# Kernel optimization log

Hardware: AMD Instinct MI355X
Metric: run time of the kernel (lower is better)

The kernel has to match this reference:

```python
import jax, jax.numpy as jnp
import numpy as np

B, M = 64, 2048
D_LLM = 4096
D_T, D_P, D_C = 256, 512, 1024
NH_T, NH_P, NH_C = 4, 8, 16
S_T, S_P, S_C = 4, 8, 4
LN_EPS = 1e-5


def setup_inputs() -> dict:
    key = jax.random.key(0)
    ks = iter(jax.random.split(key, 48))
    def n(shape, s=0.02):
        return jax.random.normal(next(ks), shape, jnp.float32) * s
    inp = {
        "hidden_state": jax.random.normal(next(ks), (B, D_LLM), jnp.float32),
        "time_fiber": jax.random.normal(next(ks), (M, D_T), jnp.float32),
        "topic_fiber": jax.random.normal(next(ks), (M, D_P), jnp.float32),
        "ctx_fiber": jax.random.normal(next(ks), (M, D_C), jnp.float32),
        "mem_mask": jnp.zeros((B, M), bool),
        # BundleQueryHeads: Linear(d_LLM -> d_F_*) per bundle (torch weight layout (out,in))
        "Wq_time": n((D_T, D_LLM)), "bq_time": jnp.zeros((D_T,), jnp.float32),
        "Wq_topic": n((D_P, D_LLM)), "bq_topic": jnp.zeros((D_P,), jnp.float32),
        "Wq_ctx": n((D_C, D_LLM)), "bq_ctx": jnp.zeros((D_C,), jnp.float32),
        # nn.MultiheadAttention packed in_proj (3d, d) and out_proj (d, d)
        "Wqkv_time": n((3 * D_T, D_T)), "bqkv_time": jnp.zeros((3 * D_T,), jnp.float32),
        "Wo_time": n((D_T, D_T)), "bo_time": jnp.zeros((D_T,), jnp.float32),
        "Wqkv_topic": n((3 * D_P, D_P)), "bqkv_topic": jnp.zeros((3 * D_P,), jnp.float32),
        "Wo_topic": n((D_P, D_P)), "bo_topic": jnp.zeros((D_P,), jnp.float32),
        "Wqkv_ctx": n((3 * D_C, D_C)), "bqkv_ctx": jnp.zeros((3 * D_C,), jnp.float32),
        "Wo_ctx": n((D_C, D_C)), "bo_ctx": jnp.zeros((D_C,), jnp.float32),
        # per-slot lifts stacked: (slots, d_F, d_LLM) for einsum 'bd,sde->bse'
        "Wlift_time": n((S_T, D_T, D_LLM)), "blift_time": jnp.zeros((S_T, D_LLM), jnp.float32),
        "Wlift_topic": n((S_P, D_P, D_LLM)), "blift_topic": jnp.zeros((S_P, D_LLM), jnp.float32),
        "Wlift_ctx": n((S_C, D_C, D_LLM)), "blift_ctx": jnp.zeros((S_C, D_LLM), jnp.float32),
        "ln_g": jnp.ones((D_LLM,), jnp.float32),
        "ln_b": jnp.zeros((D_LLM,), jnp.float32),
    }
    return inp


def _mha1(q, kv, Wqkv, bqkv, Wo, bo, nh, mask):
    """Single-query-token MHA. q: (B,d); kv: (M,d) shared across batch; mask: (B,M) True=ignore."""
    d = q.shape[-1]
    hd = d // nh
    Wq, Wk, Wv = jnp.split(Wqkv, 3, axis=0)
    bq, bk, bv = jnp.split(bqkv, 3, axis=0)
    qp = (q @ Wq.T + bq).reshape(-1, nh, hd)    # (B,h,hd)
    kp = (kv @ Wk.T + bk).reshape(-1, nh, hd)   # (M,h,hd)
    vp = (kv @ Wv.T + bv).reshape(-1, nh, hd)   # (M,h,hd)
    scale = 1.0 / np.float32(np.sqrt(hd))
    scores = jnp.einsum('bhd,mhd->bhm', qp, kp) * scale  # (B,h,M)
    scores = jnp.where(mask[:, None, :], jnp.float32(-1e9), scores)
    attn = jax.nn.softmax(scores, axis=-1)
    out = jnp.einsum('bhm,mhd->bhd', attn, vp).reshape(-1, d)  # (B,d)
    return out @ Wo.T + bo


def _layernorm(x, g, b):
    mu = jnp.mean(x, axis=-1, keepdims=True)
    var = jnp.mean((x - mu) ** 2, axis=-1, keepdims=True)
    return (x - mu) * jax.lax.rsqrt(var + LN_EPS) * g + b


def reference(hidden_state, time_fiber, topic_fiber, ctx_fiber, mem_mask,
              Wq_time, bq_time, Wq_topic, bq_topic, Wq_ctx, bq_ctx,
              Wqkv_time, bqkv_time, Wo_time, bo_time,
              Wqkv_topic, bqkv_topic, Wo_topic, bo_topic,
              Wqkv_ctx, bqkv_ctx, Wo_ctx, bo_ctx,
              Wlift_time, blift_time, Wlift_topic, blift_topic, Wlift_ctx, blift_ctx,
              ln_g, ln_b):
    # bundle query heads
    q_time = hidden_state @ Wq_time.T + bq_time
    q_topic = hidden_state @ Wq_topic.T + bq_topic
    q_ctx = hidden_state @ Wq_ctx.T + bq_ctx
    # three single-token cross attentions
    o_time = _mha1(q_time, time_fiber, Wqkv_time, bqkv_time, Wo_time, bo_time, NH_T, mem_mask)
    o_topic = _mha1(q_topic, topic_fiber, Wqkv_topic, bqkv_topic, Wo_topic, bo_topic, NH_P, mem_mask)
    o_ctx = _mha1(q_ctx, ctx_fiber, Wqkv_ctx, bqkv_ctx, Wo_ctx, bo_ctx, NH_C, mem_mask)
    # per-slot lifts, batched across slots
    slots_time = jnp.einsum('bd,sde->bse', o_time, Wlift_time) + blift_time[None]
    slots_topic = jnp.einsum('bd,sde->bse', o_topic, Wlift_topic) + blift_topic[None]
    slots_ctx = jnp.einsum('bd,sde->bse', o_ctx, Wlift_ctx) + blift_ctx[None]
    prefix = jnp.concatenate([slots_time, slots_topic, slots_ctx], axis=1)  # (B, L_mem, d_LLM)
    return _layernorm(prefix, ln_g, ln_b)
```

## Files before the change

### kernel.cpp

```cpp
#include <hip/hip_runtime.h>
#include <cstdint>
#include <cstddef>

typedef __attribute__((ext_vector_type(8))) short short8;
typedef __attribute__((ext_vector_type(4))) float floatx4;

__device__ __forceinline__ unsigned short f2bf(float f) {
    unsigned int u = __builtin_bit_cast(unsigned int, f);
    u += 0x7fffu + ((u >> 16) & 1u);
    return (unsigned short)(u >> 16);
}
__device__ __forceinline__ float bflo(unsigned int u) {
    return __builtin_bit_cast(float, u << 16);
}
__device__ __forceinline__ short8 pack8(float4 a, float4 b) {
    short8 r;
    r[0] = (short)f2bf(a.x); r[1] = (short)f2bf(a.y);
    r[2] = (short)f2bf(a.z); r[3] = (short)f2bf(a.w);
    r[4] = (short)f2bf(b.x); r[5] = (short)f2bf(b.y);
    r[6] = (short)f2bf(b.z); r[7] = (short)f2bf(b.w);
    return r;
}

struct SubGemm {
    const float* A; const float* W; const float* bias;
    float* Cf; unsigned short* Ch;
    int K, N, Kc, nj, ni, nkz, mode, ldc;
};
struct GemmBatch { SubGemm d[16]; int start[16]; int nd; };

__global__ __launch_bounds__(256) void gemm_batch(GemmBatch gb)
{
    __shared__ short As[2][64 * 40];
    __shared__ __align__(16) char Braw[2][32 * 132 * 4];

    const int bx = blockIdx.x;
    int di = 0;
#pragma unroll 1
    for (int i = 1; i < gb.nd; ++i) if (bx >= gb.start[i]) di = i;
    const SubGemm g = gb.d[di];
    int local = bx - gb.start[di];
    const int jb = local % g.nj; local /= g.nj;
    const int ib = local % g.ni;
    const int kz = local / g.ni;

    const int tid = threadIdx.x;
    const int w = tid >> 6, lane = tid & 63;
    const int quad = lane >> 4, l16 = lane & 15;
    const int noff = w * 32;

    const int rA = tid >> 2, cA = (tid & 3) * 8;
    const float* pa = g.A + (size_t)(ib * 64 + rA) * g.K + kz * g.Kc + cA;

    floatx4 acc[4][2] = {};

    if (g.mode <= 1) {
        const int rB = tid >> 1, cB = (tid & 1) * 16;
        const float* pb = g.W + (size_t)(jb * 128 + rB) * g.K + kz * g.Kc + cB;
        float4 a0 = *(const float4*)(pa), a1 = *(const float4*)(pa + 4);
        float4 b0 = *(const float4*)(pb),     b1 = *(const float4*)(pb + 4);
        float4 b2 = *(const float4*)(pb + 8), b3 = *(const float4*)(pb + 12);
        {
            short* Asp = As[0]; short* Bsp = (short*)Braw[0];
            *(short8*)&Asp[rA * 40 + cA]     = pack8(a0, a1);
            *(short8*)&Bsp[rB * 40 + cB]     = pack8(b0, b1);
            *(short8*)&Bsp[rB * 40 + cB + 8] = pack8(b2, b3);
        }
        if (g.Kc > 32) {
            pa += 32; pb += 32;
            a0 = *(const float4*)(pa);     a1 = *(const float4*)(pa + 4);
            b0 = *(const float4*)(pb);     b1 = *(const float4*)(pb + 4);
            b2 = *(const float4*)(pb + 8); b3 = *(const float4*)(pb + 12);
        }
        int cur = 0;
#pragma unroll 1
        for (int k0 = 0; k0 < g.Kc; k0 += 32) {
            __syncthreads();
            const short* Asc = As[cur];
            const short* Bsc = (const short*)Braw[cur];
            short8 af[4], bfr[2];
#pragma unroll
            for (int r = 0; r < 4; ++r)
                af[r] = *(const short8*)&Asc[(r * 16 + l16) * 40 + quad * 8];
#pragma unroll
            for (int c = 0; c < 2; ++c)
                bfr[c] = *(const short8*)&Bsc[(noff + c * 16 + l16) * 40 + quad * 8];
#pragma unroll
            for (int r = 0; r < 4; ++r)
#pragma unroll
                for (int c = 0; c < 2; ++c)
                    acc[r][c] = __builtin_amdgcn_mfma_f32_16x16x32_bf16(af[r], bfr[c], acc[r][c], 0, 0, 0);
            if (k0 + 32 < g.Kc) {
                short* Asn = As[cur ^ 1]; short* Bsn = (short*)Braw[cur ^ 1];
                *(short8*)&Asn[rA * 40 + cA]     = pack8(a0, a1);
                *(short8*)&Bsn[rB * 40 + cB]     = pack8(b0, b1);
                *(short8*)&Bsn[rB * 40 + cB + 8] = pack8(b2, b3);
                if (k0 + 64 < g.Kc) {
                    pa += 32; pb += 32;
                    a0 = *(const float4*)(pa);     a1 = *(const float4*)(pa + 4);
                    b0 = *(const float4*)(pb);     b1 = *(const float4*)(pb + 4);
                    b2 = *(const float4*)(pb + 8); b3 = *(const float4*)(pb + 12);
                }
            }
            cur ^= 1;
        }
    } else {
        const int rK = tid >> 3, cN = (tid & 7) * 16;
        const int cNs = cN ^ ((rK & 8) << 1);
        const float* pb = g.W + (size_t)(kz * g.Kc + rK) * g.N + jb * 128 + cN;
        float4 a0 = *(const float4*)(pa), a1 = *(const float4*)(pa + 4);
        float4 b0 = *(const float4*)(pb),     b1 = *(const float4*)(pb + 4);
        float4 b2 = *(const float4*)(pb + 8), b3 = *(const float4*)(pb + 12);
        {
            short* Asp = As[0]; float* Bp = (float*)Braw[0];
            *(short8*)&Asp[rA * 40 + cA] = pack8(a0, a1);
            *(float4*)&Bp[rK * 132 + cNs]      = b0;
            *(float4*)&Bp[rK * 132 + cNs + 4]  = b1;
            *(float4*)&Bp[rK * 132 + cNs + 8]  = b2;
            *(float4*)&Bp[rK * 132 + cNs + 12] = b3;
        }
        if (g.Kc > 32) {
            pa += 32; pb += (size_t)32 * g.N;
            a0 = *(const float4*)(pa);     a1 = *(const float4*)(pa + 4);
            b0 = *(const float4*)(pb);     b1 = *(const float4*)(pb + 4);
            b2 = *(const float4*)(pb + 8); b3 = *(const float4*)(pb + 12);
        }
        int cur = 0;
#pragma unroll 1
        for (int k0 = 0; k0 < g.Kc; k0 += 32) {
            __syncthreads();
            const short* Asc = As[cur];
            const float* Bc = (const float*)Braw[cur];
            short8 af[4], bfr[2];
#pragma unroll
            for (int r = 0; r < 4; ++r)
                af[r] = *(const short8*)&Asc[(r * 16 + l16) * 40 + quad * 8];
#pragma unroll
            for (int c = 0; c < 2; ++c) {
                const int colb = (noff + c * 16 + l16) ^ ((quad & 1) << 4);
#pragma unroll
                for (int i = 0; i < 8; ++i)
                    bfr[c][i] = (short)f2bf(Bc[(quad * 8 + i) * 132 + colb]);
            }
#pragma unroll
            for (int r = 0; r < 4; ++r)
#pragma unroll
                for (int c = 0; c < 2; ++c)
                    acc[r][c] = __builtin_amdgcn_mfma_f32_16x16x32_bf16(af[r], bfr[c], acc[r][c], 0, 0, 0);
            if (k0 + 32 < g.Kc) {
                short* Asn = As[cur ^ 1]; float* Bn = (float*)Braw[cur ^ 1];
                *(short8*)&Asn[rA * 40 + cA] = pack8(a0, a1);
                *(float4*)&Bn[rK * 132 + cNs]      = b0;
                *(float4*)&Bn[rK * 132 + cNs + 4]  = b1;
                *(float4*)&Bn[rK * 132 + cNs + 8]  = b2;
                *(float4*)&Bn[rK * 132 + cNs + 12] = b3;
                if (k0 + 64 < g.Kc) {
                    pa += 32; pb += (size_t)32 * g.N;
                    a0 = *(const float4*)(pa);     a1 = *(const float4*)(pa + 4);
                    b0 = *(const float4*)(pb);     b1 = *(const float4*)(pb + 4);
                    b2 = *(const float4*)(pb + 8); b3 = *(const float4*)(pb + 12);
                }
            }
            cur ^= 1;
        }
    }

#pragma unroll
    for (int r = 0; r < 4; ++r)
#pragma unroll
        for (int c = 0; c < 2; ++c) {
            const int col = jb * 128 + noff + c * 16 + l16;
            const float bj = (g.bias == nullptr) ? 0.f
                           : ((g.mode == 1 && kz != 0) ? 0.f : g.bias[col]);
#pragma unroll
            for (int q = 0; q < 4; ++q) {
                const int row = ib * 64 + r * 16 + quad * 4 + q;
                const float v = acc[r][c][q] + bj;
                if (g.mode == 0)
                    g.Ch[(size_t)row * g.ldc + col] = f2bf(v);
                else if (g.mode == 1) {
                    if (g.nkz > 1) atomicAdd(&g.Cf[(size_t)row * g.ldc + col], v);
                    else           g.Cf[(size_t)row * g.ldc + col] = v;
                } else {
                    if (g.nkz > 1) atomicAdd(&g.Cf[(size_t)row * g.ldc + col], v);
                    else           g.Cf[(size_t)row * g.ldc + col] = v;
                }
            }
        }
}

__global__ __launch_bounds__(256) void qk_batch(
    const float* __restrict__ qp_t, const float* __restrict__ qp_p, const float* __restrict__ qp_c,
    const unsigned short* __restrict__ kv_t, const unsigned short* __restrict__ kv_p, const unsigned short* __restrict__ kv_c,
    float* __restrict__ S_t, float* __restrict__ S_p, float* __restrict__ S_c)
{
    __shared__ short As[64 * 72];
    __shared__ short Bs[128 * 72];
    const int hy = blockIdx.y;
    const float* qp; const unsigned short* kv; float* S; int d, h;
    if (hy < 4)       { qp = qp_t; kv = kv_t; S = S_t; d = 256;  h = hy; }
    else if (hy < 12) { qp = qp_p; kv = kv_p; S = S_p; d = 512;  h = hy - 4; }
    else              { qp = qp_c; kv = kv_c; S = S_c; d = 1024; h = hy - 12; }

    const int j0 = blockIdx.x * 128;
    const int tid = threadIdx.x;
    const int w = tid >> 6, lane = tid & 63;
    const int quad = lane >> 4, l16 = lane & 15;
    const int noff = w * 32;
    const int twoD = 2 * d;

    {
        const int b = tid >> 2, kc = (tid & 3) * 16;
        const float* ga = qp + (size_t)b * d + h * 64 + kc;
        float4 a0 = *(const float4*)(ga + 0), a1 = *(const float4*)(ga + 4);
        float4 a2 = *(const float4*)(ga + 8), a3 = *(const float4*)(ga + 12);
        *(short8*)&As[b * 72 + kc + 0] = pack8(a0, a1);
        *(short8*)&As[b * 72 + kc + 8] = pack8(a2, a3);
    }
    {
        const int m = tid >> 1, hf = (tid & 1) * 32;
        const unsigned short* gb = kv + (size_t)(j0 + m) * twoD + h * 64 + hf;
        uint4 b0 = *(const uint4*)(gb + 0),  b1 = *(const uint4*)(gb + 8);
        uint4 b2 = *(const uint4*)(gb + 16), b3 = *(const uint4*)(gb + 24);
        *(uint4*)&Bs[m * 72 + hf + 0]  = b0;
        *(uint4*)&Bs[m * 72 + hf + 8]  = b1;
        *(uint4*)&Bs[m * 72 + hf + 16] = b2;
        *(uint4*)&Bs[m * 72 + hf + 24] = b3;
    }
    __syncthreads();

    floatx4 acc[4][2] = {};
#pragma unroll
    for (int k0 = 0; k0 < 64; k0 += 32) {
        short8 af[4], bfr[2];
#pragma unroll
        for (int r = 0; r < 4; ++r)
            af[r] = *(const short8*)&As[(r * 16 + l16) * 72 + k0 + quad * 8];
#pragma unroll
        for (int c = 0; c < 2; ++c)
            bfr[c] = *(const short8*)&Bs[(noff + c * 16 + l16) * 72 + k0 + quad * 8];
#pragma unroll
        for (int r = 0; r < 4; ++r)
#pragma unroll
            for (int c = 0; c < 2; ++c)
                acc[r][c] = __builtin_amdgcn_mfma_f32_16x16x32_bf16(af[r], bfr[c], acc[r][c], 0, 0, 0);
    }
#pragma unroll
    for (int r = 0; r < 4; ++r)
#pragma unroll
        for (int c = 0; c < 2; ++c) {
            int col = j0 + noff + c * 16 + l16;
#pragma unroll
            for (int q = 0; q < 4; ++q) {
                int row = r * 16 + quad * 4 + q;
                S[((size_t)h * 64 + row) * 2048 + col] = acc[r][c][q] * 0.125f;
            }
        }
}

__global__ __launch_bounds__(256) void softmax_pv_batch(
    const float* __restrict__ S_t, const float* __restrict__ S_p, const float* __restrict__ S_c,
    const unsigned short* __restrict__ kv_t, const unsigned short* __restrict__ kv_p, const unsigned short* __restrict__ kv_c,
    const uint8_t* __restrict__ mask,
    float* __restrict__ o_t, float* __restrict__ o_p, float* __restrict__ o_c)
{
    const int hy = blockIdx.x, b = blockIdx.y;
    const float* S; const unsigned short* kv; float* o; int d, h;
    if (hy < 4)       { S = S_t; kv = kv_t; o = o_t; d = 256;  h = hy; }
    else if (hy < 12) { S = S_p; kv = kv_p; o = o_p; d = 512;  h = hy - 4; }
    else              { S = S_c; kv = kv_c; o = o_c; d = 1024; h = hy - 12; }

    const int tid = threadIdx.x;
    __shared__ __align__(16) float sc[2048];
    __shared__ float red[4];
    __shared__ float part[4][64];
    __shared__ float s_max, s_sum;

    const float* Sr = S + ((size_t)h * 64 + b) * 2048;
    const uint8_t* mr = mask + (size_t)b * 2048;

    float lmax = -1e30f;
    for (int m = tid; m < 2048; m += 256) {
        float s = Sr[m];
        if (mr[m]) s = -1e9f;
        sc[m] = s;
        lmax = fmaxf(lmax, s);
    }
#pragma unroll
    for (int off = 32; off; off >>= 1) lmax = fmaxf(lmax, __shfl_down(lmax, off));
    if ((tid & 63) == 0) red[tid >> 6] = lmax;
    __syncthreads();
    if (tid == 0) s_max = fmaxf(fmaxf(red[0], red[1]), fmaxf(red[2], red[3]));
    __syncthreads();
    const float mx = s_max;

    float lsum = 0.f;
    for (int m = tid; m < 2048; m += 256) {
        float e = __expf(sc[m] - mx);
        sc[m] = e;
        lsum += e;
    }
#pragma unroll
    for (int off = 32; off; off >>= 1) lsum += __shfl_down(lsum, off);
    if ((tid & 63) == 0) red[tid >> 6] = lsum;
    __syncthreads();
    if (tid == 0) s_sum = red[0] + red[1] + red[2] + red[3];
    __syncthreads();

    const int lane = tid & 63, w = tid >> 6;
    const int twoD = 2 * d;
    const unsigned short* vcol = kv + d + h * 64 + lane;
    float acc = 0.f;
    const int m0 = w * 512;
#pragma unroll 1
    for (int m = m0; m < m0 + 512; m += 8) {
#pragma unroll
        for (int j = 0; j < 8; ++j)
            acc += sc[m + j] * bflo((unsigned int)vcol[(size_t)(m + j) * twoD]);
    }
    part[w][lane] = acc;
    __syncthreads();
    if (tid < 64) {
        float r = (part[0][tid] + part[1][tid] + part[2][tid] + part[3][tid]) / s_sum;
        o[(size_t)b * d + h * 64 + tid] = r;
    }
}

__global__ __launch_bounds__(256) void ln_kernel(
    float* __restrict__ x, const float* __restrict__ g, const float* __restrict__ bb,
    const float* __restrict__ blt, const float* __restrict__ blp, const float* __restrict__ blc)
{
    const int row = blockIdx.x;
    const int l = row & 15;
    const float* lb = (l < 4)  ? (blt + (size_t)l * 4096)
                    : (l < 12) ? (blp + (size_t)(l - 4) * 4096)
                               : (blc + (size_t)(l - 12) * 4096);
    float* xr = x + (size_t)row * 4096;
    const int tid = threadIdx.x;
    float v[16];
    float sum = 0.f, sumsq = 0.f;
#pragma unroll
    for (int i = 0; i < 16; ++i) {
        int e = tid + i * 256;
        v[i] = xr[e] + lb[e];
        sum += v[i];
        sumsq += v[i] * v[i];
    }
    __shared__ float rs[4], rq[4];
#pragma unroll
    for (int off = 32; off; off >>= 1) {
        sum += __shfl_down(sum, off);
        sumsq += __shfl_down(sumsq, off);
    }
    if ((tid & 63) == 0) { rs[tid >> 6] = sum; rq[tid >> 6] = sumsq; }
    __syncthreads();
    const float ts = rs[0] + rs[1] + rs[2] + rs[3];
    const float tq = rq[0] + rq[1] + rq[2] + rq[3];
    const float mu = ts * (1.f / 4096.f);
    const float var = tq * (1.f / 4096.f) - mu * mu;
    const float r = rsqrtf(var + 1e-5f);
#pragma unroll
    for (int i = 0; i < 16; ++i) {
        int e = tid + i * 256;
        xr[e] = (v[i] - mu) * r * g[e] + bb[e];
    }
}

static void addg(GemmBatch& G, int& tot,
                 const float* A, const float* W, const float* bias,
                 float* Cf, unsigned short* Ch,
                 int K, int N, int Kc, int nj, int ni, int nkz, int mode, int ldc)
{
    SubGemm& s = G.d[G.nd];
    s.A = A; s.W = W; s.bias = bias; s.Cf = Cf; s.Ch = Ch;
    s.K = K; s.N = N; s.Kc = Kc; s.nj = nj; s.ni = ni; s.nkz = nkz;
    s.mode = mode; s.ldc = ldc;
    G.start[G.nd] = tot;
    tot += nj * ni * nkz;
    G.nd++;
}

extern "C" void kernel_launch(void* const* d_in, const int* in_sizes, int n_in,
                              void* d_out, int out_size, void* d_ws, size_t ws_size,
                              hipStream_t stream)
{
    const float*   hs     = (const float*)d_in[0];
    const float*   fib_t  = (const float*)d_in[1];
    const float*   fib_p  = (const float*)d_in[2];
    const float*   fib_c  = (const float*)d_in[3];
    const uint8_t* mask   = (const uint8_t*)d_in[4];
    const float* Wq_t   = (const float*)d_in[5];  const float* bq_t   = (const float*)d_in[6];
    const float* Wq_p   = (const float*)d_in[7];  const float* bq_p   = (const float*)d_in[8];
    const float* Wq_c   = (const float*)d_in[9];  const float* bq_c   = (const float*)d_in[10];
    const float* Wqkv_t = (const float*)d_in[11]; const float* bqkv_t = (const float*)d_in[12];
    const float* Wo_t   = (const float*)d_in[13]; const float* bo_t   = (const float*)d_in[14];
    const float* Wqkv_p = (const float*)d_in[15]; const float* bqkv_p = (const float*)d_in[16];
    const float* Wo_p   = (const float*)d_in[17]; const float* bo_p   = (const float*)d_in[18];
    const float* Wqkv_c = (const float*)d_in[19]; const float* bqkv_c = (const float*)d_in[20];
    const float* Wo_c   = (const float*)d_in[21]; const float* bo_c   = (const float*)d_in[22];
    const float* Wl_t   = (const float*)d_in[23]; const float* bl_t   = (const float*)d_in[24];
    const float* Wl_p   = (const float*)d_in[25]; const float* bl_p   = (const float*)d_in[26];
    const float* Wl_c   = (const float*)d_in[27]; const float* bl_c   = (const float*)d_in[28];
    const float* ln_g   = (const float*)d_in[29]; const float* ln_b   = (const float*)d_in[30];

    char* wsb = (char*)d_ws;
    float* q_t  = (float*)wsb; wsb += 64 * 256 * 4;
    float* q_p  = (float*)wsb; wsb += 64 * 512 * 4;
    float* q_c  = (float*)wsb; wsb += 64 * 1024 * 4;
    float* qp_t = (float*)wsb; wsb += 64 * 256 * 4;
    float* qp_p = (float*)wsb; wsb += 64 * 512 * 4;
    float* qp_c = (float*)wsb; wsb += 64 * 1024 * 4;
    float* po_t = (float*)wsb; wsb += 64 * 256 * 4;
    float* po_p = (float*)wsb; wsb += 64 * 512 * 4;
    float* po_c = (float*)wsb; wsb += 64 * 1024 * 4;
    size_t zbytes = (size_t)(wsb - (char*)d_ws);
    float* o_t  = (float*)wsb; wsb += 64 * 256 * 4;
    float* o_p  = (float*)wsb; wsb += 64 * 512 * 4;
    float* o_c  = (float*)wsb; wsb += 64 * 1024 * 4;
    unsigned short* kv_t = (unsigned short*)wsb; wsb += 2048 * 512 * 2;
    unsigned short* kv_p = (unsigned short*)wsb; wsb += 2048 * 1024 * 2;
    unsigned short* kv_c = (unsigned short*)wsb; wsb += 2048 * 2048 * 2;
    float* S_t = (float*)wsb; wsb += (size_t)4  * 64 * 2048 * 4;
    float* S_p = (float*)wsb; wsb += (size_t)8  * 64 * 2048 * 4;
    float* S_c = (float*)wsb; wsb += (size_t)16 * 64 * 2048 * 4;
    float* out = (float*)d_out;

    const dim3 blk(256);
    hipMemsetAsync(d_ws, 0, zbytes, stream);
    hipMemsetAsync(d_out, 0, (size_t)out_size, stream);

    {
        GemmBatch G{}; int tot = 0; G.nd = 0;
        addg(G, tot, fib_c, Wqkv_c + 1024 * 1024, bqkv_c + 1024, nullptr, kv_c, 1024, 2048, 1024, 16, 32, 1, 0, 2048);
        addg(G, tot, fib_p, Wqkv_p + 512 * 512,   bqkv_p + 512,  nullptr, kv_p, 512,  1024, 512,  8,  32, 1, 0, 1024);
        addg(G, tot, fib_t, Wqkv_t + 256 * 256,   bqkv_t + 256,  nullptr, kv_t, 256,  512,  256,  4,  32, 1, 0, 512);
        addg(G, tot, hs, Wq_c, bq_c, q_c, nullptr, 4096, 1024, 256, 8, 1, 16, 1, 1024);
        addg(G, tot, hs, Wq_p, bq_p, q_p, nullptr, 4096, 512,  256, 4, 1, 16, 1, 512);
        addg(G, tot, hs, Wq_t, bq_t, q_t, nullptr, 4096, 256,  256, 2, 1, 16, 1, 256);
        gemm_batch<<<dim3(tot), blk, 0, stream>>>(G);
    }

    {
        GemmBatch G{}; int tot = 0; G.nd = 0;
        addg(G, tot, q_c, Wqkv_c, bqkv_c, qp_c, nullptr, 1024, 1024, 128, 8, 1, 8, 1, 1024);
        addg(G, tot, q_p, Wqkv_p, bqkv_p, qp_p, nullptr, 512,  512,  64,  4, 1, 8, 1, 512);
        addg(G, tot, q_t, Wqkv_t, bqkv_t, qp_t, nullptr, 256,  256,  64,  2, 1, 4, 1, 256);
        gemm_batch<<<dim3(tot), blk, 0, stream>>>(G);
    }

    qk_batch<<<dim3(16, 28), blk, 0, stream>>>(qp_t, qp_p, qp_c, kv_t, kv_p, kv_c, S_t, S_p, S_c);
    softmax_pv_batch<<<dim3(28, 64), blk, 0, stream>>>(S_t, S_p, S_c, kv_t, kv_p, kv_c, mask, o_t, o_p, o_c);

    {
        GemmBatch G{}; int tot = 0; G.nd = 0;
        addg(G, tot, o_c, Wo_c, bo_c, po_c, nullptr, 1024, 1024, 128, 8, 1, 8, 1, 1024);
        addg(G, tot, o_p, Wo_p, bo_p, po_p, nullptr, 512,  512,  64,  4, 1, 8, 1, 512);
        addg(G, tot, o_t, Wo_t, bo_t, po_t, nullptr, 256,  256,  64,  2, 1, 4, 1, 256);
        gemm_batch<<<dim3(tot), blk, 0, stream>>>(G);
    }

    {
        GemmBatch G{}; int tot = 0; G.nd = 0;
        for (int z = 0; z < 4; ++z)
            addg(G, tot, po_c, Wl_c + (size_t)z * 1024 * 4096, nullptr,
                 out + (size_t)(12 + z) * 4096, nullptr, 1024, 4096, 256, 32, 1, 4, 2, 16 * 4096);
        for (int z = 0; z < 8; ++z)
            addg(G, tot, po_p, Wl_p + (size_t)z * 512 * 4096, nullptr,
                 out + (size_t)(4 + z) * 4096, nullptr, 512, 4096, 256, 32, 1, 2, 2, 16 * 4096);
        for (int z = 0; z < 4; ++z)
            addg(G, tot, po_t, Wl_t + (size_t)z * 256 * 4096, nullptr,
                 out + (size_t)z * 4096, nullptr, 256, 4096, 256, 32, 1, 1, 2, 16 * 4096);
        gemm_batch<<<dim3(tot), blk, 0, stream>>>(G);
    }

    ln_kernel<<<dim3(1024), blk, 0, stream>>>(out, ln_g, ln_b, bl_t, bl_p, bl_c);
}
```

Baseline: 402.0 us.

## Split KV projection into 128x128 tiled GEMM and load B fragments directly to registers

The KV projection of the fibers moves out of the batched 64x128 GEMM into a dedicated 128x128-tile kernel with XOR-swizzled LDS, which doubles operand reuse per block. The thin GEMMs (query heads, in/out projections, lifts) no longer stage the weight matrix through shared memory. Each lane loads its B fragment straight from global memory into registers, with two-step software pipelining, which drops the B LDS traffic and its padding. The trade-offs are uncoalesced strided global loads for the transposed-weight mode, an extra kernel launch, and more registers per thread.

Measured after the change: 407.1 us. About the same (+1.3%).

```diff
diff --git a/kernel.cpp b/kernel.cpp
--- a/kernel.cpp
+++ b/kernel.cpp
@@ -24,15 +24,21 @@
 
 struct SubGemm {
     const float* A; const float* W; const float* bias;
-    float* Cf; unsigned short* Ch;
+    float* Cf;
     int K, N, Kc, nj, ni, nkz, mode, ldc;
 };
 struct GemmBatch { SubGemm d[16]; int start[16]; int nd; };
 
+#define MFMA_ALL() { _Pragma("unroll") for (int r_ = 0; r_ < 4; ++r_) { \
+    acc[r_][0] = __builtin_amdgcn_mfma_f32_16x16x32_bf16(af[r_], bfr0, acc[r_][0], 0, 0, 0); \
+    acc[r_][1] = __builtin_amdgcn_mfma_f32_16x16x32_bf16(af[r_], bfr1, acc[r_][1], 0, 0, 0); } }
+
+#define READ_AF(buf) { _Pragma("unroll") for (int r_ = 0; r_ < 4; ++r_) \
+    af[r_] = *(const short8*)&As[buf][aoff[r_]]; }
+
 __global__ __launch_bounds__(256) void gemm_batch(GemmBatch gb)
 {
     __shared__ short As[2][64 * 40];
-    __shared__ __align__(16) char Braw[2][32 * 132 * 4];
 
     const int bx = blockIdx.x;
     int di = 0;
@@ -49,119 +55,108 @@
     const int quad = lane >> 4, l16 = lane & 15;
     const int noff = w * 32;
 
-    const int rA = tid >> 2, cA = (tid & 3) * 8;
-    const float* pa = g.A + (size_t)(ib * 64 + rA) * g.K + kz * g.Kc + cA;
+    const int rA = tid >> 2;
+    const int sAs = rA * 40 + (((tid & 3) ^ ((rA >> 3) & 3)) << 3);
+    const float* pa = g.A + (size_t)(ib * 64 + rA) * g.K + kz * g.Kc + (tid & 3) * 8;
+
+    int aoff[4];
+#pragma unroll
+    for (int r = 0; r < 4; ++r) {
+        int row = r * 16 + l16;
+        aoff[r] = row * 40 + ((quad ^ ((row >> 3) & 3)) << 3);
+    }
 
     floatx4 acc[4][2] = {};
-
-    if (g.mode <= 1) {
-        const int rB = tid >> 1, cB = (tid & 1) * 16;
-        const float* pb = g.W + (size_t)(jb * 128 + rB) * g.K + kz * g.Kc + cB;
-        float4 a0 = *(const float4*)(pa), a1 = *(const float4*)(pa + 4);
-        float4 b0 = *(const float4*)(pb),     b1 = *(const float4*)(pb + 4);
-        float4 b2 = *(const float4*)(pb + 8), b3 = *(const float4*)(pb + 12);
-        {
-            short* Asp = As[0]; short* Bsp = (short*)Braw[0];
-            *(short8*)&Asp[rA * 40 + cA]     = pack8(a0, a1);
-            *(short8*)&Bsp[rB * 40 + cB]     = pack8(b0, b1);
-            *(short8*)&Bsp[rB * 40 + cB + 8] = pack8(b2, b3);
-        }
-        if (g.Kc > 32) {
-            pa += 32; pb += 32;
-            a0 = *(const float4*)(pa);     a1 = *(const float4*)(pa + 4);
-            b0 = *(const float4*)(pb);     b1 = *(const float4*)(pb + 4);
-            b2 = *(const float4*)(pb + 8); b3 = *(const float4*)(pb + 12);
-        }
-        int cur = 0;
+    const int steps = g.Kc >> 5;
+    short8 af[4], bfr0, bfr1;
+
+    if (g.mode == 1) {
+        const float* q0 = g.W + (size_t)(jb * 128 + noff + l16) * g.K + kz * g.Kc + quad * 8;
+        const float* q1 = q0 + (size_t)16 * g.K;
+        float4 xa0, xa1, ya0, ya1;
+        float4 xb0, xb1, xb2, xb3, yb0, yb1, yb2, yb3;
+        xa0 = *(const float4*)pa;        xa1 = *(const float4*)(pa + 4);
+        xb0 = *(const float4*)q0;        xb1 = *(const float4*)(q0 + 4);
+        xb2 = *(const float4*)q1;        xb3 = *(const float4*)(q1 + 4);
+        pa += 32; q0 += 32; q1 += 32;
+        ya0 = *(const float4*)pa;        ya1 = *(const float4*)(pa + 4);
+        yb0 = *(const float4*)q0;        yb1 = *(const float4*)(q0 + 4);
+        yb2 = *(const float4*)q1;        yb3 = *(const float4*)(q1 + 4);
+        pa += 32; q0 += 32; q1 += 32;
+        *(short8*)&As[0][sAs] = pack8(xa0, xa1);
 #pragma unroll 1
-        for (int k0 = 0; k0 < g.Kc; k0 += 32) {
+        for (int s = 0; s < steps; s += 2) {
             __syncthreads();
-            const short* Asc = As[cur];
-            const short* Bsc = (const short*)Braw[cur];
-            short8 af[4], bfr[2];
-#pragma unroll
-            for (int r = 0; r < 4; ++r)
-                af[r] = *(const short8*)&Asc[(r * 16 + l16) * 40 + quad * 8];
-#pragma unroll
-            for (int c = 0; c < 2; ++c)
-                bfr[c] = *(const short8*)&Bsc[(noff + c * 16 + l16) * 40 + quad * 8];
-#pragma unroll
-            for (int r = 0; r < 4; ++r)
-#pragma unroll
-                for (int c = 0; c < 2; ++c)
-                    acc[r][c] = __builtin_amdgcn_mfma_f32_16x16x32_bf16(af[r], bfr[c], acc[r][c], 0, 0, 0);
-            if (k0 + 32 < g.Kc) {
-                short* Asn = As[cur ^ 1]; short* Bsn = (short*)Braw[cur ^ 1];
-                *(short8*)&Asn[rA * 40 + cA]     = pack8(a0, a1);
-                *(short8*)&Bsn[rB * 40 + cB]     = pack8(b0, b1);
-                *(short8*)&Bsn[rB * 40 + cB + 8] = pack8(b2, b3);
-                if (k0 + 64 < g.Kc) {
-                    pa += 32; pb += 32;
-                    a0 = *(const float4*)(pa);     a1 = *(const float4*)(pa + 4);
-                    b0 = *(const float4*)(pb);     b1 = *(const float4*)(pb + 4);
-                    b2 = *(const float4*)(pb + 8); b3 = *(const float4*)(pb + 12);
+            READ_AF(0);
+            bfr0 = pack8(xb0, xb1); bfr1 = pack8(xb2, xb3);
+            MFMA_ALL();
+            *(short8*)&As[1][sAs] = pack8(ya0, ya1);
+            if (s + 2 < steps) {
+                xa0 = *(const float4*)pa; xa1 = *(const float4*)(pa + 4);
+                xb0 = *(const float4*)q0; xb1 = *(const float4*)(q0 + 4);
+                xb2 = *(const float4*)q1; xb3 = *(const float4*)(q1 + 4);
+                pa += 32; q0 += 32; q1 += 32;
+            }
+            __syncthreads();
+            READ_AF(1);
+            bfr0 = pack8(yb0, yb1); bfr1 = pack8(yb2, yb3);
+            MFMA_ALL();
+            if (s + 2 < steps) {
+                *(short8*)&As[0][sAs] = pack8(xa0, xa1);
+                if (s + 3 < steps) {
+                    ya0 = *(const float4*)pa; ya1 = *(const float4*)(pa + 4);
+                    yb0 = *(const float4*)q0; yb1 = *(const float4*)(q0 + 4);
+                    yb2 = *(const float4*)q1; yb3 = *(const float4*)(q1 + 4);
+                    pa += 32; q0 += 32; q1 += 32;
                 }
             }
-            cur ^= 1;
         }
     } else {
-        const int rK = tid >> 3, cN = (tid & 7) * 16;
-        const int cNs = cN ^ ((rK & 8) << 1);
-        const float* pb = g.W + (size_t)(kz * g.Kc + rK) * g.N + jb * 128 + cN;
-        float4 a0 = *(const float4*)(pa), a1 = *(const float4*)(pa + 4);
-        float4 b0 = *(const float4*)(pb),     b1 = *(const float4*)(pb + 4);
-        float4 b2 = *(const float4*)(pb + 8), b3 = *(const float4*)(pb + 12);
-        {
-            short* Asp = As[0]; float* Bp = (float*)Braw[0];
-            *(short8*)&Asp[rA * 40 + cA] = pack8(a0, a1);
-            *(float4*)&Bp[rK * 132 + cNs]      = b0;
-            *(float4*)&Bp[rK * 132 + cNs + 4]  = b1;
-            *(float4*)&Bp[rK * 132 + cNs + 8]  = b2;
-            *(float4*)&Bp[rK * 132 + cNs + 12] = b3;
-        }
-        if (g.Kc > 32) {
-            pa += 32; pb += (size_t)32 * g.N;
-            a0 = *(const float4*)(pa);     a1 = *(const float4*)(pa + 4);
-            b0 = *(const float4*)(pb);     b1 = *(const float4*)(pb + 4);
-            b2 = *(const float4*)(pb + 8); b3 = *(const float4*)(pb + 12);
-        }
-        int cur = 0;
+        const float* rp[8];
+#pragma unroll
+        for (int i = 0; i < 8; ++i)
+            rp[i] = g.W + ((size_t)(kz * g.Kc) + quad * 8 + i) * g.N
+                        + (jb * 128 + noff + l16);
+        const size_t bstep = (size_t)32 * g.N;
+        float xnb[16], ynb[16];
+        float4 xa0, xa1, ya0, ya1;
+
+#define LDB_X() { _Pragma("unroll") for (int i_ = 0; i_ < 8; ++i_) { \
+        xnb[i_] = rp[i_][0]; xnb[8 + i_] = rp[i_][16]; rp[i_] += bstep; } }
+#define LDB_Y() { _Pragma("unroll") for (int i_ = 0; i_ < 8; ++i_) { \
+        ynb[i_] = rp[i_][0]; ynb[8 + i_] = rp[i_][16]; rp[i_] += bstep; } }
+#define CVT_X() { _Pragma("unroll") for (int e_ = 0; e_ < 8; ++e_) { \
+        bfr0[e_] = (short)f2bf(xnb[e_]); bfr1[e_] = (short)f2bf(xnb[8 + e_]); } }
+#define CVT_Y() { _Pragma("unroll") for (int e_ = 0; e_ < 8; ++e_) { \
+        bfr0[e_] = (short)f2bf(ynb[e_]); bfr1[e_] = (short)f2bf(ynb[8 + e_]); } }
+
+        xa0 = *(const float4*)pa; xa1 = *(const float4*)(pa + 4); pa += 32;
+        LDB_X();
+        ya0 = *(const float4*)pa; ya1 = *(const float4*)(pa + 4); pa += 32;
+        LDB_Y();
+        *(short8*)&As[0][sAs] = pack8(xa0, xa1);
 #pragma unroll 1
-        for (int k0 = 0; k0 < g.Kc; k0 += 32) {
+        for (int s = 0; s < steps; s += 2) {
             __syncthreads();
-            const short* Asc = As[cur];
-            const float* Bc = (const float*)Braw[cur];
-            short8 af[4], bfr[2];
-#pragma unroll
-            for (int r = 0; r < 4; ++r)
-                af[r] = *(const short8*)&Asc[(r * 16 + l16) * 40 + quad * 8];
-#pragma unroll
-            for (int c = 0; c < 2; ++c) {
-                const int colb = (noff + c * 16 + l16) ^ ((quad & 1) << 4);
-#pragma unroll
-                for (int i = 0; i < 8; ++i)
-                    bfr[c][i] = (short)f2bf(Bc[(quad * 8 + i) * 132 + colb]);
-            }
-#pragma unroll
-            for (int r = 0; r < 4; ++r)
-#pragma unroll
-                for (int c = 0; c < 2; ++c)
-                    acc[r][c] = __builtin_amdgcn_mfma_f32_16x16x32_bf16(af[r], bfr[c], acc[r][c], 0, 0, 0);
-            if (k0 + 32 < g.Kc) {
-                short* Asn = As[cur ^ 1]; float* Bn = (float*)Braw[cur ^ 1];
-                *(short8*)&Asn[rA * 40 + cA] = pack8(a0, a1);
-                *(float4*)&Bn[rK * 132 + cNs]      = b0;
-                *(float4*)&Bn[rK * 132 + cNs + 4]  = b1;
-                *(float4*)&Bn[rK * 132 + cNs + 8]  = b2;
-                *(float4*)&Bn[rK * 132 + cNs + 12] = b3;
-                if (k0 + 64 < g.Kc) {
-                    pa += 32; pb += (size_t)32 * g.N;
-                    a0 = *(const float4*)(pa);     a1 = *(const float4*)(pa + 4);
-                    b0 = *(const float4*)(pb);     b1 = *(const float4*)(pb + 4);
-                    b2 = *(const float4*)(pb + 8); b3 = *(const float4*)(pb + 12);
+            READ_AF(0);
+            CVT_X();
+            MFMA_ALL();
+            *(short8*)&As[1][sAs] = pack8(ya0, ya1);
+            if (s + 2 < steps) {
+                xa0 = *(const float4*)pa; xa1 = *(const float4*)(pa + 4); pa += 32;
+                LDB_X();
+            }
+            __syncthreads();
+            READ_AF(1);
+            CVT_Y();
+            MFMA_ALL();
+            if (s + 2 < steps) {
+                *(short8*)&As[0][sAs] = pack8(xa0, xa1);
+                if (s + 3 < steps) {
+                    ya0 = *(const float4*)pa; ya1 = *(const float4*)(pa + 4); pa += 32;
+                    LDB_Y();
                 }
             }
-            cur ^= 1;
         }
     }
 
@@ -170,21 +165,113 @@
 #pragma unroll
         for (int c = 0; c < 2; ++c) {
             const int col = jb * 128 + noff + c * 16 + l16;
-            const float bj = (g.bias == nullptr) ? 0.f
-                           : ((g.mode == 1 && kz != 0) ? 0.f : g.bias[col]);
+            const float bj = (g.bias != nullptr && kz == 0) ? g.bias[col] : 0.f;
 #pragma unroll
             for (int q = 0; q < 4; ++q) {
                 const int row = ib * 64 + r * 16 + quad * 4 + q;
                 const float v = acc[r][c][q] + bj;
-                if (g.mode == 0)
-                    g.Ch[(size_t)row * g.ldc + col] = f2bf(v);
-                else if (g.mode == 1) {
-                    if (g.nkz > 1) atomicAdd(&g.Cf[(size_t)row * g.ldc + col], v);
-                    else           g.Cf[(size_t)row * g.ldc + col] = v;
-                } else {
-                    if (g.nkz > 1) atomicAdd(&g.Cf[(size_t)row * g.ldc + col], v);
-                    else           g.Cf[(size_t)row * g.ldc + col] = v;
-                }
+                if (g.nkz > 1) atomicAdd(&g.Cf[(size_t)row * g.ldc + col], v);
+                else           g.Cf[(size_t)row * g.ldc + col] = v;
+            }
+        }
+}
+
+struct Sub128 { const float* A; const float* W; const float* bias; unsigned short* C; int K, N, nj; };
+struct Batch128 { Sub128 d[4]; int start[4]; int nd; };
+
+__global__ __launch_bounds__(256) void gemm128(Batch128 gb)
+{
+    __shared__ short As[2][128 * 40];
+    __shared__ short Bs[2][128 * 40];
+
+    const int bx = blockIdx.x;
+    int di = 0;
+#pragma unroll 1
+    for (int i = 1; i < gb.nd; ++i) if (bx >= gb.start[i]) di = i;
+    const Sub128 g = gb.d[di];
+    const int local = bx - gb.start[di];
+    const int jb = local % g.nj, ib = local / g.nj;
+
+    const int tid = threadIdx.x;
+    const int w = tid >> 6, lane = tid & 63;
+    const int quad = lane >> 4, l16 = lane & 15;
+    const int wm = (w >> 1) * 64, wn = (w & 1) * 64;
+
+    const int rS = tid >> 1;
+    const int gi0 = (tid & 1) * 2;
+    const int jsw = (rS >> 3) & 3;
+    const int s1 = rS * 40 + ((gi0 ^ jsw) << 3);
+    const int s2 = rS * 40 + (((gi0 + 1) ^ jsw) << 3);
+    const float* pa = g.A + (size_t)(ib * 128 + rS) * g.K + (tid & 1) * 16;
+    const float* pb = g.W + (size_t)(jb * 128 + rS) * g.K + (tid & 1) * 16;
+
+    int aoff[4], boff[4];
+#pragma unroll
+    for (int r = 0; r < 4; ++r) {
+        int rowA = wm + r * 16 + l16;
+        aoff[r] = rowA * 40 + ((quad ^ ((rowA >> 3) & 3)) << 3);
+        int rowB = wn + r * 16 + l16;
+        boff[r] = rowB * 40 + ((quad ^ ((rowB >> 3) & 3)) << 3);
+    }
+
+    floatx4 acc[4][4] = {};
+    float4 a0 = *(const float4*)pa,       a1 = *(const float4*)(pa + 4);
+    float4 a2 = *(const float4*)(pa + 8), a3 = *(const float4*)(pa + 12);
+    float4 b0 = *(const float4*)pb,       b1 = *(const float4*)(pb + 4);
+    float4 b2 = *(const float4*)(pb + 8), b3 = *(const float4*)(pb + 12);
+    *(short8*)&As[0][s1] = pack8(a0, a1);
+    *(short8*)&As[0][s2] = pack8(a2, a3);
+    *(short8*)&Bs[0][s1] = pack8(b0, b1);
+    *(short8*)&Bs[0][s2] = pack8(b2, b3);
+    if (g.K > 32) {
+        pa += 32; pb += 32;
+        a0 = *(const float4*)pa;       a1 = *(const float4*)(pa + 4);
+        a2 = *(const float4*)(pa + 8); a3 = *(const float4*)(pa + 12);
+        b0 = *(const float4*)pb;       b1 = *(const float4*)(pb + 4);
+        b2 = *(const float4*)(pb + 8); b3 = *(const float4*)(pb + 12);
+    }
+    int cur = 0;
+#pragma unroll 1
+    for (int k0 = 0; k0 < g.K; k0 += 32) {
+        __syncthreads();
+        short8 af[4], bf[4];
+#pragma unroll
+        for (int r = 0; r < 4; ++r) {
+            af[r] = *(const short8*)&As[cur][aoff[r]];
+            bf[r] = *(const short8*)&Bs[cur][boff[r]];
+        }
+#pragma unroll
+        for (int r = 0; r < 4; ++r)
+#pragma unroll
+            for (int c = 0; c < 4; ++c)
+                acc[r][c] = __builtin_amdgcn_mfma_f32_16x16x32_bf16(af[r], bf[c], acc[r][c], 0, 0, 0);
+        if (k0 + 32 < g.K) {
+            short* An = As[cur ^ 1]; short* Bn = Bs[cur ^ 1];
+            *(short8*)&An[s1] = pack8(a0, a1);
+            *(short8*)&An[s2] = pack8(a2, a3);
+            *(short8*)&Bn[s1] = pack8(b0, b1);
+            *(short8*)&Bn[s2] = pack8(b2, b3);
+            if (k0 + 64 < g.K) {
+                pa += 32; pb += 32;
+                a0 = *(const float4*)pa;       a1 = *(const float4*)(pa + 4);
+                a2 = *(const float4*)(pa + 8); a3 = *(const float4*)(pa + 12);
+                b0 = *(const float4*)pb;       b1 = *(const float4*)(pb + 4);
+                b2 = *(const float4*)(pb + 8); b3 = *(const float4*)(pb + 12);
+            }
+        }
+        cur ^= 1;
+    }
+
+#pragma unroll
+    for (int r = 0; r < 4; ++r)
+#pragma unroll
+        for (int c = 0; c < 4; ++c) {
+            const int col = jb * 128 + wn + c * 16 + l16;
+            const float bj = g.bias[col];
+#pragma unroll
+            for (int q = 0; q < 4; ++q) {
+                const int row = ib * 128 + wm + r * 16 + quad * 4 + q;
+                g.C[(size_t)row * g.N + col] = f2bf(acc[r][c][q] + bj);
             }
         }
 }
@@ -367,16 +454,25 @@
 }
 
 static void addg(GemmBatch& G, int& tot,
-                 const float* A, const float* W, const float* bias,
-                 float* Cf, unsigned short* Ch,
+                 const float* A, const float* W, const float* bias, float* Cf,
                  int K, int N, int Kc, int nj, int ni, int nkz, int mode, int ldc)
 {
     SubGemm& s = G.d[G.nd];
-    s.A = A; s.W = W; s.bias = bias; s.Cf = Cf; s.Ch = Ch;
+    s.A = A; s.W = W; s.bias = bias; s.Cf = Cf;
     s.K = K; s.N = N; s.Kc = Kc; s.nj = nj; s.ni = ni; s.nkz = nkz;
     s.mode = mode; s.ldc = ldc;
     G.start[G.nd] = tot;
     tot += nj * ni * nkz;
+    G.nd++;
+}
+static void add128(Batch128& G, int& tot,
+                   const float* A, const float* W, const float* bias, unsigned short* C,
+                   int K, int N, int nj, int ni)
+{
+    Sub128& s = G.d[G.nd];
+    s.A = A; s.W = W; s.bias = bias; s.C = C; s.K = K; s.N = N; s.nj = nj;
+    G.start[G.nd] = tot;
+    tot += nj * ni;
     G.nd++;
 }
 
@@ -431,20 +527,25 @@
 
     {
         GemmBatch G{}; int tot = 0; G.nd = 0;
-        addg(G, tot, fib_c, Wqkv_c + 1024 * 1024, bqkv_c + 1024, nullptr, kv_c, 1024, 2048, 1024, 16, 32, 1, 0, 2048);
-        addg(G, tot, fib_p, Wqkv_p + 512 * 512,   bqkv_p + 512,  nullptr, kv_p, 512,  1024, 512,  8,  32, 1, 0, 1024);
-        addg(G, tot, fib_t, Wqkv_t + 256 * 256,   bqkv_t + 256,  nullptr, kv_t, 256,  512,  256,  4,  32, 1, 0, 512);
-        addg(G, tot, hs, Wq_c, bq_c, q_c, nullptr, 4096, 1024, 256, 8, 1, 16, 1, 1024);
-        addg(G, tot, hs, Wq_p, bq_p, q_p, nullptr, 4096, 512,  256, 4, 1, 16, 1, 512);
-        addg(G, tot, hs, Wq_t, bq_t, q_t, nullptr, 4096, 256,  256, 2, 1, 16, 1, 256);
+        addg(G, tot, hs, Wq_c, bq_c, q_c, 4096, 1024, 256, 8, 1, 16, 1, 1024);
+        addg(G, tot, hs, Wq_p, bq_p, q_p, 4096, 512,  256, 4, 1, 16, 1, 512);
+        addg(G, tot, hs, Wq_t, bq_t, q_t, 4096, 256,  256, 2, 1, 16, 1, 256);
         gemm_batch<<<dim3(tot), blk, 0, stream>>>(G);
     }
 
     {
+        Batch128 G{}; int tot = 0; G.nd = 0;
+        add128(G, tot, fib_c, Wqkv_c + 1024 * 1024, bqkv_c + 1024, kv_c, 1024, 2048, 16, 16);
+        add128(G, tot, fib_p, Wqkv_p + 512 * 512,   bqkv_p + 512,  kv_p, 512,  1024, 8,  16);
+        add128(G, tot, fib_t, Wqkv_t + 256 * 256,   bqkv_t + 256,  kv_t, 256,  512,  4,  16);
+        gemm128<<<dim3(tot), blk, 0, stream>>>(G);
+    }
+
+    {
         GemmBatch G{}; int tot = 0; G.nd = 0;
-        addg(G, tot, q_c, Wqkv_c, bqkv_c, qp_c, nullptr, 1024, 1024, 128, 8, 1, 8, 1, 1024);
-        addg(G, tot, q_p, Wqkv_p, bqkv_p, qp_p, nullptr, 512,  512,  64,  4, 1, 8, 1, 512);
-        addg(G, tot, q_t, Wqkv_t, bqkv_t, qp_t, nullptr, 256,  256,  64,  2, 1, 4, 1, 256);
+        addg(G, tot, q_c, Wqkv_c, bqkv_c, qp_c, 1024, 1024, 128, 8, 1, 8, 1, 1024);
+        addg(G, tot, q_p, Wqkv_p, bqkv_p, qp_p, 512,  512,  64,  4, 1, 8, 1, 512);
+        addg(G, tot, q_t, Wqkv_t, bqkv_t, qp_t, 256,  256,  64,  2, 1, 4, 1, 256);
         gemm_batch<<<dim3(tot), blk, 0, stream>>>(G);
     }
 
@@ -453,9 +554,9 @@
 
     {
         GemmBatch G{}; int tot = 0; G.nd = 0;
-        addg(G, tot, o_c, Wo_c, bo_c, po_c, nullptr, 1024, 1024, 128, 8, 1, 8, 1, 1024);
-        addg(G, tot, o_p, Wo_p, bo_p, po_p, nullptr, 512,  512,  64,  4, 1, 8, 1, 512);
-        addg(G, tot, o_t, Wo_t, bo_t, po_t, nullptr, 256,  256,  64,  2, 1, 4, 1, 256);
+        addg(G, tot, o_c, Wo_c, bo_c, po_c, 1024, 1024, 128, 8, 1, 8, 1, 1024);
+        addg(G, tot, o_p, Wo_p, bo_p, po_p, 512,  512,  64,  4, 1, 8, 1, 512);
+        addg(G, tot, o_t, Wo_t, bo_t, po_t, 256,  256,  64,  2, 1, 4, 1, 256);
         gemm_batch<<<dim3(tot), blk, 0, stream>>>(G);
     }
 
@@ -463,13 +564,13 @@
         GemmBatch G{}; int tot = 0; G.nd = 0;
         for (int z = 0; z < 4; ++z)
             addg(G, tot, po_c, Wl_c + (size_t)z * 1024 * 4096, nullptr,
-                 out + (size_t)(12 + z) * 4096, nullptr, 1024, 4096, 256, 32, 1, 4, 2, 16 * 4096);
+                 out + (size_t)(12 + z) * 4096, 1024, 4096, 256, 32, 1, 4, 2, 16 * 4096);
         for (int z = 0; z < 8; ++z)
             addg(G, tot, po_p, Wl_p + (size_t)z * 512 * 4096, nullptr,
-                 out + (size_t)(4 + z) * 4096, nullptr, 512, 4096, 256, 32, 1, 2, 2, 16 * 4096);
+                 out + (size_t)(4 + z) * 4096, 512, 4096, 256, 32, 1, 2, 2, 16 * 4096);
         for (int z = 0; z < 4; ++z)
             addg(G, tot, po_t, Wl_t + (size_t)z * 256 * 4096, nullptr,
-                 out + (size_t)z * 4096, nullptr, 256, 4096, 256, 32, 1, 1, 2, 16 * 4096);
+                 out + (size_t)z * 4096, 256, 4096, 256, 32, 1, 1, 2, 16 * 4096);
         gemm_batch<<<dim3(tot), blk, 0, stream>>>(G);
     }
 
```
